# Kernel tuning notes

Hardware: AMD Instinct MI355X
Metric: run time of the kernel (lower is better)

The kernel has to match this reference:

```python
import jax, jax.numpy as jnp
import numpy as np

INPUT_SZ = 1024
HIDDEN_SZ = 1024


def setup_inputs() -> dict:
    key = jax.random.key(0)
    k1, k2, k3, k4, k5, k6 = jax.random.split(key, 6)
    s = 1.0 / np.sqrt(INPUT_SZ)
    x_batch = jax.random.normal(k1, (8, 2048, INPUT_SZ), dtype=jnp.float32)
    lin_w = jax.random.normal(k2, (INPUT_SZ, INPUT_SZ), dtype=jnp.float32) * s  # nn.Linear weight (out,in)
    lin_b = jax.random.normal(k3, (INPUT_SZ,), dtype=jnp.float32) * s
    W_q = jax.random.normal(k4, (INPUT_SZ, HIDDEN_SZ), dtype=jnp.float32) * s
    W_k = jax.random.normal(k5, (INPUT_SZ, HIDDEN_SZ), dtype=jnp.float32) * s
    W_v = jax.random.normal(k6, (INPUT_SZ, HIDDEN_SZ), dtype=jnp.float32) * s
    return {"x_batch": x_batch, "lin_w": lin_w, "lin_b": lin_b,
            "W_q": W_q, "W_k": W_k, "W_v": W_v}


def reference(x_batch, lin_w, lin_b, W_q, W_k, W_v):
    # x_batch: [B, S, D]. Prefill path (empty kv_cache of shape (2,)).
    B, S, D = x_batch.shape
    x = jnp.einsum('bsd,ed->bse', x_batch, lin_w) + lin_b  # nn.Linear: x @ W.T + b
    Q = jnp.einsum('bsd,dh->bsh', x, W_q)
    K = jnp.einsum('bsd,dh->bsh', x, W_k)
    V = jnp.einsum('bsd,dh->bsh', x, W_v)
    current_cache = jnp.stack([K, V])  # [2, B, S, H]
    I = jnp.einsum('bqh,bkh->bqk', Q, K)  # NOTE: no 1/sqrt(d) scaling, per original
    causal_mask = jnp.triu(jnp.ones((S, S), dtype=bool), k=1)  # True above diagonal
    I = jnp.where(causal_mask[None, :, :], -jnp.inf, I)
    F = jnp.einsum('bqk,bkh->bqh', jax.nn.softmax(I, axis=-1), V)
    return (F, current_cache)
```

## Files before the change

kernel.cpp:

```cpp
#include <hip/hip_runtime.h>
#include <cstdint>
#include <cstddef>


typedef short bf16x8 __attribute__((ext_vector_type(8)));
typedef float f32x4 __attribute__((ext_vector_type(4)));

__device__ __forceinline__ unsigned short f2bf(float f) {
    unsigned u = __float_as_uint(f);
    return (unsigned short)((u + 0x7fffu + ((u >> 16) & 1u)) >> 16);
}
__device__ __forceinline__ float bf2f(unsigned short h) {
    return __uint_as_float(((unsigned)h) << 16);
}

#define GLDS(gp, lp)                                                                \
    __builtin_amdgcn_global_load_lds((const __attribute__((address_space(1))) void*)(gp), \
                                     (__attribute__((address_space(3))) void*)(lp), 16, 0, 0)

#define PACK_BATCH ((size_t)136 * 16384)


__global__ __launch_bounds__(256)
void cvt_split(const float* __restrict__ in, unsigned short* __restrict__ h,
               unsigned short* __restrict__ l, size_t n4)
{
    size_t i = (size_t)blockIdx.x * blockDim.x + threadIdx.x;
    size_t stride = (size_t)gridDim.x * blockDim.x;
    for (; i < n4; i += stride) {
        float4 v = ((const float4*)in)[i];
        unsigned short h0 = f2bf(v.x), h1 = f2bf(v.y), h2 = f2bf(v.z), h3 = f2bf(v.w);
        uint2 hp, lp;
        hp.x = (unsigned)h0 | ((unsigned)h1 << 16);
        hp.y = (unsigned)h2 | ((unsigned)h3 << 16);
        lp.x = (unsigned)f2bf(v.x - bf2f(h0)) | ((unsigned)f2bf(v.y - bf2f(h1)) << 16);
        lp.y = (unsigned)f2bf(v.z - bf2f(h2)) | ((unsigned)f2bf(v.w - bf2f(h3)) << 16);
        ((uint2*)h)[i] = hp;
        ((uint2*)l)[i] = lp;
    }
}

template<bool PAIR>
__global__ __launch_bounds__(256)
void cvt_split_T(const float* __restrict__ in, unsigned short* __restrict__ hT,
                 unsigned short* __restrict__ lT, int R, int C,
                 size_t inBatch, size_t outBatch)
{
    __shared__ float tile[64][65];
    in += (size_t)blockIdx.z * inBatch;
    hT += (size_t)blockIdx.z * outBatch;
    const int c0 = blockIdx.x * 64, r0 = blockIdx.y * 64;
    const int tx = threadIdx.x & 63, ty = threadIdx.x >> 6;
    for (int i = ty; i < 64; i += 4)
        tile[i][tx] = in[(size_t)(r0 + i) * C + c0 + tx];
    __syncthreads();
    for (int i = ty; i < 64; i += 4) {
        float v = tile[tx][i];
        unsigned short hh = f2bf(v);
        size_t off = (size_t)(c0 + i) * R + r0 + tx;
        hT[off] = hh;
        if (PAIR) (lT + (size_t)blockIdx.z * outBatch)[off] = f2bf(v - bf2f(hh));
    }
}


template<bool SPLIT, bool BIAS, bool CMASK, bool CK, bool OUTF, bool OUTH, bool OUTL,
         bool PACKC, bool PACKA>
__global__ __launch_bounds__(256)
void gemm_bf16(const unsigned short* __restrict__ Ah, const unsigned short* __restrict__ Al,
               const unsigned short* __restrict__ Bh, const unsigned short* __restrict__ Bl,
               const float* __restrict__ bias,
               float* __restrict__ C, float* __restrict__ C7,
               unsigned short* __restrict__ Ch, unsigned short* __restrict__ Cl,
               int K, int ldA, int ldB, int ldC,
               size_t aBatch, size_t bBatch, size_t cBatch)
{
    const int row0 = blockIdx.y * 128, col0 = blockIdx.x * 128;
    if (CMASK && col0 > row0 + 127) return;

    const int bz = blockIdx.z;
    if (aBatch) { Ah += (size_t)bz * aBatch; if (SPLIT) Al += (size_t)bz * aBatch; }
    if (bBatch) { Bh += (size_t)bz * bBatch; if (SPLIT) Bl += (size_t)bz * bBatch; }
    if (cBatch) { C += (size_t)bz * cBatch; }

    extern __shared__ __align__(16) unsigned short sm[];
    unsigned short* sAh = sm;
    unsigned short* sBh = sm + 4096;
    unsigned short* sAl = sm + 8192;
    unsigned short* sBl = sm + 12288;

    const int t = threadIdx.x;
    const int wave = t >> 6, lane = t & 63;
    const int wr = wave >> 1, wc = wave & 1;
    const int mrow = lane & 15, kg = lane >> 4;

    int kEnd = K;
    if (CK) kEnd = min(K, row0 + 128);

    f32x4 acc[4][4] = {};

    const int c0 = wave * 2, c1 = wave * 2 + 1;
    size_t aOff0, aOff1;
    if (PACKA) {
        const int rblk = row0 >> 7;
        const size_t baseA = (((size_t)bz * 136) + (size_t)((rblk * (rblk + 1)) >> 1)) << 14;
        aOff0 = baseA + (size_t)(c0 * 16 + mrow) * 128 + kg * 8;
        aOff1 = baseA + (size_t)(c1 * 16 + mrow) * 128 + kg * 8;
    } else {
        aOff0 = (size_t)(row0 + c0 * 16 + mrow) * ldA + kg * 8;
        aOff1 = (size_t)(row0 + c1 * 16 + mrow) * ldA + kg * 8;
    }
    const size_t bOff0 = (size_t)(col0 + c0 * 16 + mrow) * ldB + kg * 8;
    const size_t bOff1 = (size_t)(col0 + c1 * 16 + mrow) * ldB + kg * 8;

    for (int k0 = 0; k0 < kEnd; k0 += 32) {
        const size_t aK = PACKA ? ((((size_t)(k0 >> 7)) << 14) | (size_t)(k0 & 127))
                                : (size_t)k0;
        GLDS(Ah + aOff0 + aK, sAh + c0 * 512);
        GLDS(Ah + aOff1 + aK, sAh + c1 * 512);
        GLDS(Bh + bOff0 + k0, sBh + c0 * 512);
        GLDS(Bh + bOff1 + k0, sBh + c1 * 512);
        if (SPLIT) {
            GLDS(Al + aOff0 + aK, sAl + c0 * 512);
            GLDS(Al + aOff1 + aK, sAl + c1 * 512);
            GLDS(Bl + bOff0 + k0, sBl + c0 * 512);
            GLDS(Bl + bOff1 + k0, sBl + c1 * 512);
        }
        __syncthreads();

        bf16x8 afh[4], bfh[4], afl[4], bfl[4];
        #pragma unroll
        for (int i = 0; i < 4; ++i) {
            afh[i] = *(const bf16x8*)(sAh + (wr * 4 + i) * 512 + lane * 8);
            bfh[i] = *(const bf16x8*)(sBh + (wc * 4 + i) * 512 + lane * 8);
            if (SPLIT) {
                afl[i] = *(const bf16x8*)(sAl + (wr * 4 + i) * 512 + lane * 8);
                bfl[i] = *(const bf16x8*)(sBl + (wc * 4 + i) * 512 + lane * 8);
            }
        }
        #pragma unroll
        for (int i = 0; i < 4; ++i)
            #pragma unroll
            for (int j = 0; j < 4; ++j) {
                acc[i][j] = __builtin_amdgcn_mfma_f32_16x16x32_bf16(afh[i], bfh[j], acc[i][j], 0, 0, 0);
                if (SPLIT) {
                    acc[i][j] = __builtin_amdgcn_mfma_f32_16x16x32_bf16(afh[i], bfl[j], acc[i][j], 0, 0, 0);
                    acc[i][j] = __builtin_amdgcn_mfma_f32_16x16x32_bf16(afl[i], bfh[j], acc[i][j], 0, 0, 0);
                }
            }
        __syncthreads();
    }

    float* Cout = C;
    size_t cbase = 0;
    if (PACKC) {
        const int rblk = row0 >> 7, cblk = col0 >> 7;
        Cout = (bz == 7) ? C7 : C + (size_t)bz * PACK_BATCH;
        cbase = ((size_t)((rblk * (rblk + 1)) >> 1) + (size_t)cblk) << 14;
    }
    const int rb = (lane >> 4) * 4;
    const int cl = lane & 15;
    #pragma unroll
    for (int j = 0; j < 4; ++j) {
        const int col = col0 + wc * 64 + j * 16 + cl;
        float bv = BIAS ? bias[col] : 0.f;
        #pragma unroll
        for (int i = 0; i < 4; ++i) {
            const int rw = row0 + wr * 64 + i * 16 + rb;
            #pragma unroll
            for (int r = 0; r < 4; ++r) {
                const int row = rw + r;
                float v = acc[i][j][r];
                if (BIAS) v += bv;
                if (CMASK && col > row) v = -__builtin_huge_valf();
                const size_t off = PACKC
                    ? (cbase + (size_t)(row - row0) * 128 + (size_t)(col - col0))
                    : ((size_t)row * ldC + col);
                if (OUTF) Cout[off] = v;
                if (OUTH) {
                    unsigned short hh = f2bf(v);
                    Ch[off] = hh;
                    if (OUTL) Cl[off] = f2bf(v - bf2f(hh));
                }
            }
        }
    }
}

__global__ __launch_bounds__(256)
void softmax_p_packed(const float* __restrict__ SF, const float* __restrict__ S7,
                      unsigned short* __restrict__ P)
{
    const int q = blockIdx.x, b = blockIdx.y;
    const int rblk = q >> 7, tri = (rblk * (rblk + 1)) >> 1;
    const size_t rowoff = ((size_t)tri << 14) + (size_t)(q & 127) * 128;
    const float* rowb = ((b == 7) ? S7 : SF + (size_t)b * PACK_BATCH) + rowoff;
    unsigned short* prow = P + (size_t)b * PACK_BATCH + rowoff;
    const int kend = rblk * 128 + 128;
    const int t = threadIdx.x;
    __shared__ float red[4];

    float m = -__builtin_huge_valf();
    for (int k = t; k < kend; k += 256)
        m = fmaxf(m, rowb[(((size_t)(k >> 7)) << 14) + (k & 127)]);
    #pragma unroll
    for (int off = 32; off; off >>= 1) m = fmaxf(m, __shfl_down(m, off, 64));
    if ((t & 63) == 0) red[t >> 6] = m;
    __syncthreads();
    m = fmaxf(fmaxf(red[0], red[1]), fmaxf(red[2], red[3]));
    __syncthreads();

    float e[8];
    float s = 0.f;
    int i = 0;
    for (int k = t; k < kend; k += 256, ++i) {
        float v = __expf(rowb[(((size_t)(k >> 7)) << 14) + (k & 127)] - m);
        e[i] = v;
        s += v;
    }
    #pragma unroll
    for (int off = 32; off; off >>= 1) s += __shfl_down(s, off, 64);
    if ((t & 63) == 0) red[t >> 6] = s;
    __syncthreads();
    s = red[0] + red[1] + red[2] + red[3];
    const float inv = 1.0f / s;
    i = 0;
    for (int k = t; k < kend; k += 256, ++i)
        prow[(((size_t)(k >> 7)) << 14) + (k & 127)] = f2bf(e[i] * inv);
}

#define TILE 64
#define KT 16
#define LDP (TILE + 4)
template<bool BT, bool BIAS, bool CMASK, bool CK>
__global__ __launch_bounds__(256)
void gemm_f32(const float* __restrict__ A, const float* __restrict__ B,
              const float* __restrict__ bias, float* __restrict__ C,
              int M, int N, int K, size_t sA, size_t sB, size_t sC)
{
    const int bm = blockIdx.y, bn = blockIdx.x;
    const int row0 = bm * TILE, col0 = bn * TILE;
    if (CMASK && col0 > row0 + (TILE - 1)) return;
    A += (size_t)blockIdx.z * sA; B += (size_t)blockIdx.z * sB; C += (size_t)blockIdx.z * sC;
    __shared__ float As[KT][LDP];
    __shared__ float Bs[KT][LDP];
    const int t = threadIdx.x;
    const int tx = t & 15, ty = t >> 4;
    const int lm = t >> 2, lk = (t & 3) << 2;
    int kEnd = K;
    if (CK) kEnd = min(K, row0 + TILE);
    float acc[4][4] = {};
    for (int k0 = 0; k0 < kEnd; k0 += KT) {
        {
            float4 a = *(const float4*)(A + (size_t)(row0 + lm) * K + (k0 + lk));
            As[lk + 0][lm] = a.x; As[lk + 1][lm] = a.y; As[lk + 2][lm] = a.z; As[lk + 3][lm] = a.w;
        }
        if (BT) {
            float4 b = *(const float4*)(B + (size_t)(col0 + lm) * K + (k0 + lk));
            Bs[lk + 0][lm] = b.x; Bs[lk + 1][lm] = b.y; Bs[lk + 2][lm] = b.z; Bs[lk + 3][lm] = b.w;
        } else {
            const int bk = t >> 4, bn4 = (t & 15) << 2;
            *(float4*)&Bs[bk][bn4] = *(const float4*)(B + (size_t)(k0 + bk) * N + (col0 + bn4));
        }
        __syncthreads();
        #pragma unroll
        for (int kk = 0; kk < KT; ++kk) {
            float av[4], bv[4];
            *(float4*)av = *(const float4*)&As[kk][ty << 2];
            *(float4*)bv = *(const float4*)&Bs[kk][tx << 2];
            #pragma unroll
            for (int i = 0; i < 4; ++i)
                #pragma unroll
                for (int j = 0; j < 4; ++j) acc[i][j] = fmaf(av[i], bv[j], acc[i][j]);
        }
        __syncthreads();
    }
    #pragma unroll
    for (int i = 0; i < 4; ++i) {
        const int r = row0 + (ty << 2) + i;
        float4 o; float* po = &o.x;
        #pragma unroll
        for (int j = 0; j < 4; ++j) {
            const int c = col0 + (tx << 2) + j;
            float v = acc[i][j];
            if (BIAS) v += bias[c];
            if (CMASK && c > r) v = -__builtin_huge_valf();
            po[j] = v;
        }
        *(float4*)(C + (size_t)r * N + col0 + (tx << 2)) = o;
    }
}
__global__ __launch_bounds__(256)
void softmax_causal(float* __restrict__ Sc, size_t batchStride, int ncols)
{
    const int q = blockIdx.x;
    float* row = Sc + (size_t)blockIdx.y * batchStride + (size_t)q * ncols;
    const int kend = (q & ~63) + 64;
    const int t = threadIdx.x;
    __shared__ float red[4];
    float m = -__builtin_huge_valf();
    for (int k = t; k < kend; k += 256) m = fmaxf(m, row[k]);
    #pragma unroll
    for (int off = 32; off; off >>= 1) m = fmaxf(m, __shfl_down(m, off, 64));
    if ((t & 63) == 0) red[t >> 6] = m;
    __syncthreads();
    m = fmaxf(fmaxf(red[0], red[1]), fmaxf(red[2], red[3]));
    __syncthreads();
    float e[8]; float s = 0.f; int i = 0;
    for (int k = t; k < kend; k += 256, ++i) { float v = __expf(row[k] - m); e[i] = v; s += v; }
    #pragma unroll
    for (int off = 32; off; off >>= 1) s += __shfl_down(s, off, 64);
    if ((t & 63) == 0) red[t >> 6] = s;
    __syncthreads();
    s = red[0] + red[1] + red[2] + red[3];
    const float inv = 1.0f / s;
    i = 0;
    for (int k = t; k < kend; k += 256, ++i) row[k] = e[i] * inv;
}


extern "C" void kernel_launch(void* const* d_in, const int* in_sizes, int n_in,
                              void* d_out, int out_size, void* d_ws, size_t ws_size,
                              hipStream_t stream)
{
    const float* x_batch = (const float*)d_in[0];
    const float* lin_w   = (const float*)d_in[1];
    const float* lin_b   = (const float*)d_in[2];
    const float* W_q     = (const float*)d_in[3];
    const float* W_k     = (const float*)d_in[4];
    const float* W_v     = (const float*)d_in[5];

    constexpr int Bn = 8, S = 2048, D = 1024;
    constexpr size_t MS = (size_t)Bn * S;
    constexpr size_t NE = MS * (size_t)D;
    constexpr size_t SB = (size_t)S * D;

    float* out = (float*)d_out;
    float* Fo = out;
    float* Kc = out + NE;
    float* Vc = out + 2 * NE;

    const size_t needFast = NE * 2 * 2ull
                          + NE * 2 * 2ull
                          + 14680064ull;

    if (ws_size >= needFast) {
        unsigned short* Qh  = (unsigned short*)d_ws;
        unsigned short* Ql  = Qh + NE;
        unsigned short* Kh  = Ql + NE;
        unsigned short* Kl  = Kh + NE;
        unsigned short* X   = Kl + NE;
        unsigned short* lwh = X,            *lwl = X + 1048576;
        unsigned short* wqh = X + 2097152,  *wql = X + 3145728;
        unsigned short* wkh = X + 4194304,  *wkl = X + 5242880;
        unsigned short* wvh = X + 6291456;
        float*          S7f = (float*)X;
        float*          SF  = Fo;
        unsigned short* Ph  = Qh;
        unsigned short* VhT = Kh;

        unsigned short* xbh = (unsigned short*)Kc;
        unsigned short* xbl = xbh + NE;
        unsigned short* xh  = (unsigned short*)Fo;
        unsigned short* xl  = xh + NE;

        const dim3 blk(256);

        cvt_split<<<4096, blk, 0, stream>>>(x_batch, xbh, xbl, NE / 4);
        cvt_split<<<512,  blk, 0, stream>>>(lin_w, lwh, lwl, (size_t)D * D / 4);
        cvt_split_T<true ><<<dim3(16, 16, 1), blk, 0, stream>>>(W_q, wqh, wql, D, D, 0, 0);
        cvt_split_T<true ><<<dim3(16, 16, 1), blk, 0, stream>>>(W_k, wkh, wkl, D, D, 0, 0);
        cvt_split_T<false><<<dim3(16, 16, 1), blk, 0, stream>>>(W_v, wvh, nullptr, D, D, 0, 0);

        const dim3 gBig(D / 128, MS / 128);

        gemm_bf16<true, true, false, false, false, true, true, false, false>
            <<<gBig, blk, 32768, stream>>>(xbh, xbl, lwh, lwl, lin_b,
                                           nullptr, nullptr, xh, xl, D, D, D, D, 0, 0, 0);
        gemm_bf16<true, false, false, false, false, true, true, false, false>
            <<<gBig, blk, 32768, stream>>>(xh, xl, wqh, wql, nullptr,
                                           nullptr, nullptr, Qh, Ql, D, D, D, D, 0, 0, 0);
        gemm_bf16<true, false, false, false, true, true, true, false, false>
            <<<gBig, blk, 32768, stream>>>(xh, xl, wkh, wkl, nullptr,
                                           Kc, nullptr, Kh, Kl, D, D, D, D, 0, 0, 0);
        gemm_bf16<false, false, false, false, true, false, false, false, false>
            <<<gBig, blk, 16384, stream>>>(xh, nullptr, wvh, nullptr, nullptr,
                                           Vc, nullptr, nullptr, nullptr, D, D, D, D, 0, 0, 0);

        gemm_bf16<true, false, true, false, true, false, false, true, false>
            <<<dim3(S / 128, S / 128, Bn), blk, 32768, stream>>>(
                Qh, Ql, Kh, Kl, nullptr,
                SF, S7f, nullptr, nullptr, D, D, D, 128, SB, SB, 0);

        softmax_p_packed<<<dim3(S, Bn), blk, 0, stream>>>(SF, S7f, Ph);

        cvt_split_T<false><<<dim3(D / 64, S / 64, Bn), blk, 0, stream>>>(
            Vc, VhT, nullptr, S, D, SB, SB);

        gemm_bf16<false, false, false, true, true, false, false, false, true>
            <<<dim3(D / 128, S / 128, Bn), blk, 16384, stream>>>(
                Ph, nullptr, VhT, nullptr, nullptr,
                Fo, nullptr, nullptr, nullptr, S, 128, S, D, 0, SB, SB);
    } else {
        float* x  = Fo;
        float* Q  = (float*)d_ws;
        float* Sc = Q + NE;
        const dim3 blk(256);
        const dim3 gBig(D / TILE, MS / TILE, 1);
        gemm_f32<true, true, false, false><<<gBig, blk, 0, stream>>>(
            x_batch, lin_w, lin_b, x, (int)MS, D, D, 0, 0, 0);
        gemm_f32<false, false, false, false><<<gBig, blk, 0, stream>>>(
            x, W_q, nullptr, Q, (int)MS, D, D, 0, 0, 0);
        gemm_f32<false, false, false, false><<<gBig, blk, 0, stream>>>(
            x, W_k, nullptr, Kc, (int)MS, D, D, 0, 0, 0);
        gemm_f32<false, false, false, false><<<gBig, blk, 0, stream>>>(
            x, W_v, nullptr, Vc, (int)MS, D, D, 0, 0, 0);
        for (int b = 0; b < Bn; ++b) {
            const float* Qb = Q  + (size_t)b * SB;
            const float* Kb = Kc + (size_t)b * SB;
            const float* Vb = Vc + (size_t)b * SB;
            float*       Fb = Fo + (size_t)b * SB;
            gemm_f32<true, false, true, false><<<dim3(S / TILE, S / TILE, 1), blk, 0, stream>>>(
                Qb, Kb, nullptr, Sc, S, S, D, 0, 0, 0);
            softmax_causal<<<dim3(S, 1, 1), blk, 0, stream>>>(Sc, 0, S);
            gemm_f32<false, false, false, true><<<dim3(D / TILE, S / TILE, 1), blk, 0, stream>>>(
                Sc, Vb, nullptr, Fb, S, D, S, 0, 0, 0);
        }
    }
}
```

Measured before the change: 1.247 ms.

## Add 256x256-tile GEMM kernel with triangular QK^T grid and XCD-aware block mapping

Introduces a new gemm256 kernel with 512 threads per block and 256x256 output tiles, double-buffered LDS staged via global_load_lds, and uses it for the input linear, the Q/K/V projections and the masked QK^T scores. The QK^T launch covers only lower-triangular tiles through a 1D grid decoded with a sqrt-based triangle index, and the projection GEMMs remap block IDs so consecutive tiles spread across chiplet groups. Larger tiles raise operand reuse per LDS load, but grids drop to 256 or 288 blocks, which may underfill the device. Each block also needs up to 128 KB of static shared memory and a large accumulator array, which adds register pressure.

Result: faster. 1.063 ms (-14.8%).

```diff
diff --git a/kernel.cpp b/kernel.cpp
--- a/kernel.cpp
+++ b/kernel.cpp
@@ -1,6 +1,7 @@
 #include <hip/hip_runtime.h>
 #include <cstdint>
 #include <cstddef>
+#include <cmath>
 
 
 typedef short bf16x8 __attribute__((ext_vector_type(8)));
@@ -64,6 +65,138 @@
 }
 
 
+template<bool SPLIT, bool BIAS, bool QKT, bool OUTF, bool OUTH, bool OUTL>
+__global__ __launch_bounds__(512, 2)
+void gemm256(const unsigned short* __restrict__ Ah, const unsigned short* __restrict__ Al,
+             const unsigned short* __restrict__ Bh, const unsigned short* __restrict__ Bl,
+             const float* __restrict__ bias,
+             float* __restrict__ C, float* __restrict__ C7,
+             unsigned short* __restrict__ Ch, unsigned short* __restrict__ Cl,
+             int K, int ldA, int ldB, int ldC, int nbx,
+             size_t aBatch, size_t bBatch)
+{
+    int row0, col0, batch = 0;
+    if (QKT) {
+        const int bid = blockIdx.x;
+        batch = bid & 7;
+        const int ti = bid >> 3;
+        int r = (int)((sqrtf(8.f * (float)ti + 1.f) - 1.f) * 0.5f);
+        while (((r + 1) * (r + 2)) / 2 <= ti) ++r;
+        while ((r * (r + 1)) / 2 > ti) --r;
+        const int c = ti - (r * (r + 1)) / 2;
+        row0 = r * 256; col0 = c * 256;
+        Ah += (size_t)batch * aBatch; Bh += (size_t)batch * bBatch;
+        if (SPLIT) { Al += (size_t)batch * aBatch; Bl += (size_t)batch * bBatch; }
+    } else {
+        const int bid = blockIdx.x;
+        const int chunk = gridDim.x >> 3;
+        const int lb = (bid & 7) * chunk + (bid >> 3);
+        row0 = (lb / nbx) * 256; col0 = (lb % nbx) * 256;
+    }
+
+    constexpr int PL = 8192;
+    constexpr int BUF = SPLIT ? 32768 : 16384;
+    __shared__ unsigned short sm[SPLIT ? 65536 : 32768];
+
+    const int t = threadIdx.x, wave = t >> 6, lane = t & 63;
+    const int wr = wave >> 2, wc = wave & 3;
+    const int mrow = lane & 15, kg = lane >> 4;
+    const int c0 = wave * 2, c1 = wave * 2 + 1;
+
+    const size_t aOff0 = (size_t)(row0 + c0 * 16 + mrow) * ldA + kg * 8;
+    const size_t aOff1 = (size_t)(row0 + c1 * 16 + mrow) * ldA + kg * 8;
+    const size_t bOff0 = (size_t)(col0 + c0 * 16 + mrow) * ldB + kg * 8;
+    const size_t bOff1 = (size_t)(col0 + c1 * 16 + mrow) * ldB + kg * 8;
+
+    f32x4 acc[8][4] = {};
+    const int nt = K / 32;
+
+#define STAGE256(step, bb)                                                   \
+    do {                                                                     \
+        unsigned short* db = sm + (bb);                                      \
+        const size_t kof = (size_t)(step) * 32;                              \
+        GLDS(Ah + aOff0 + kof, db + c0 * 512);                               \
+        GLDS(Ah + aOff1 + kof, db + c1 * 512);                               \
+        GLDS(Bh + bOff0 + kof, db + (SPLIT ? 2 * PL : PL) + c0 * 512);       \
+        GLDS(Bh + bOff1 + kof, db + (SPLIT ? 2 * PL : PL) + c1 * 512);       \
+        if (SPLIT) {                                                         \
+            GLDS(Al + aOff0 + kof, db + PL + c0 * 512);                      \
+            GLDS(Al + aOff1 + kof, db + PL + c1 * 512);                      \
+            GLDS(Bl + bOff0 + kof, db + 3 * PL + c0 * 512);                  \
+            GLDS(Bl + bOff1 + kof, db + 3 * PL + c1 * 512);                  \
+        }                                                                    \
+    } while (0)
+
+    STAGE256(0, 0);
+    __syncthreads();
+
+    for (int ts = 0; ts < nt; ++ts) {
+        unsigned short* sb = sm + (ts & 1) * BUF;
+        if (ts + 1 < nt) STAGE256(ts + 1, ((ts + 1) & 1) * BUF);
+        bf16x8 bh[4], bl[4];
+        #pragma unroll
+        for (int j = 0; j < 4; ++j) {
+            bh[j] = *(const bf16x8*)(sb + (SPLIT ? 2 * PL : PL) + (wc * 4 + j) * 512 + lane * 8);
+            if (SPLIT) bl[j] = *(const bf16x8*)(sb + 3 * PL + (wc * 4 + j) * 512 + lane * 8);
+        }
+        #pragma unroll
+        for (int i = 0; i < 8; ++i) {
+            bf16x8 ah = *(const bf16x8*)(sb + (wr * 8 + i) * 512 + lane * 8);
+            bf16x8 al;
+            if (SPLIT) al = *(const bf16x8*)(sb + PL + (wr * 8 + i) * 512 + lane * 8);
+            __builtin_amdgcn_s_setprio(1);
+            #pragma unroll
+            for (int j = 0; j < 4; ++j) {
+                acc[i][j] = __builtin_amdgcn_mfma_f32_16x16x32_bf16(ah, bh[j], acc[i][j], 0, 0, 0);
+                if (SPLIT) {
+                    acc[i][j] = __builtin_amdgcn_mfma_f32_16x16x32_bf16(ah, bl[j], acc[i][j], 0, 0, 0);
+                    acc[i][j] = __builtin_amdgcn_mfma_f32_16x16x32_bf16(al, bh[j], acc[i][j], 0, 0, 0);
+                }
+            }
+            __builtin_amdgcn_s_setprio(0);
+        }
+        __syncthreads();
+    }
+#undef STAGE256
+
+    float* Cout = C;
+    if (QKT) Cout = (batch == 7) ? C7 : C + (size_t)batch * PACK_BATCH;
+    const int rb = (lane >> 4) * 4, cl = lane & 15;
+    #pragma unroll
+    for (int j = 0; j < 4; ++j) {
+        const int col = col0 + wc * 64 + j * 16 + cl;
+        const float bv = BIAS ? bias[col] : 0.f;
+        #pragma unroll
+        for (int i = 0; i < 8; ++i) {
+            const int rw = row0 + wr * 128 + i * 16 + rb;
+            #pragma unroll
+            for (int r = 0; r < 4; ++r) {
+                const int row = rw + r;
+                float v = acc[i][j][r];
+                if (BIAS) v += bv;
+                if (QKT) {
+                    if (col > row) v = -__builtin_huge_valf();
+                    const int rblk = row >> 7, cblk = col >> 7;
+                    if (rblk >= cblk) {
+                        const size_t off = ((size_t)(((rblk * (rblk + 1)) >> 1) + cblk) << 14)
+                                         + ((size_t)(row & 127) << 7) + (size_t)(col & 127);
+                        Cout[off] = v;
+                    }
+                } else {
+                    const size_t off = (size_t)row * ldC + col;
+                    if (OUTF) Cout[off] = v;
+                    if (OUTH) {
+                        unsigned short hh = f2bf(v);
+                        Ch[off] = hh;
+                        if (OUTL) Cl[off] = f2bf(v - bf2f(hh));
+                    }
+                }
+            }
+        }
+    }
+}
+
+
 template<bool SPLIT, bool BIAS, bool CMASK, bool CK, bool OUTF, bool OUTH, bool OUTL,
          bool PACKC, bool PACKA>
 __global__ __launch_bounds__(256)
@@ -83,11 +216,11 @@
     if (bBatch) { Bh += (size_t)bz * bBatch; if (SPLIT) Bl += (size_t)bz * bBatch; }
     if (cBatch) { C += (size_t)bz * cBatch; }
 
-    extern __shared__ __align__(16) unsigned short sm[];
-    unsigned short* sAh = sm;
-    unsigned short* sBh = sm + 4096;
-    unsigned short* sAl = sm + 8192;
-    unsigned short* sBl = sm + 12288;
+    extern __shared__ __align__(16) unsigned short smd[];
+    unsigned short* sAh = smd;
+    unsigned short* sBh = smd + 4096;
+    unsigned short* sAl = smd + 8192;
+    unsigned short* sBl = smd + 12288;
 
     const int t = threadIdx.x;
     const int wave = t >> 6, lane = t & 63;
@@ -365,6 +498,7 @@
         unsigned short* xl  = xh + NE;
 
         const dim3 blk(256);
+        const dim3 blk512(512);
 
         cvt_split<<<4096, blk, 0, stream>>>(x_batch, xbh, xbl, NE / 4);
         cvt_split<<<512,  blk, 0, stream>>>(lin_w, lwh, lwl, (size_t)D * D / 4);
@@ -372,25 +506,19 @@
         cvt_split_T<true ><<<dim3(16, 16, 1), blk, 0, stream>>>(W_k, wkh, wkl, D, D, 0, 0);
         cvt_split_T<false><<<dim3(16, 16, 1), blk, 0, stream>>>(W_v, wvh, nullptr, D, D, 0, 0);
 
-        const dim3 gBig(D / 128, MS / 128);
-
-        gemm_bf16<true, true, false, false, false, true, true, false, false>
-            <<<gBig, blk, 32768, stream>>>(xbh, xbl, lwh, lwl, lin_b,
-                                           nullptr, nullptr, xh, xl, D, D, D, D, 0, 0, 0);
-        gemm_bf16<true, false, false, false, false, true, true, false, false>
-            <<<gBig, blk, 32768, stream>>>(xh, xl, wqh, wql, nullptr,
-                                           nullptr, nullptr, Qh, Ql, D, D, D, D, 0, 0, 0);
-        gemm_bf16<true, false, false, false, true, true, true, false, false>
-            <<<gBig, blk, 32768, stream>>>(xh, xl, wkh, wkl, nullptr,
-                                           Kc, nullptr, Kh, Kl, D, D, D, D, 0, 0, 0);
-        gemm_bf16<false, false, false, false, true, false, false, false, false>
-            <<<gBig, blk, 16384, stream>>>(xh, nullptr, wvh, nullptr, nullptr,
-                                           Vc, nullptr, nullptr, nullptr, D, D, D, D, 0, 0, 0);
-
-        gemm_bf16<true, false, true, false, true, false, false, true, false>
-            <<<dim3(S / 128, S / 128, Bn), blk, 32768, stream>>>(
-                Qh, Ql, Kh, Kl, nullptr,
-                SF, S7f, nullptr, nullptr, D, D, D, 128, SB, SB, 0);
+        gemm256<true, true, false, false, true, true><<<dim3(256), blk512, 0, stream>>>(
+            xbh, xbl, lwh, lwl, lin_b, nullptr, nullptr, xh, xl, D, D, D, D, 4, 0, 0);
+        gemm256<true, false, false, false, true, true><<<dim3(256), blk512, 0, stream>>>(
+            xh, xl, wqh, wql, nullptr, nullptr, nullptr, Qh, Ql, D, D, D, D, 4, 0, 0);
+        gemm256<true, false, false, true, true, true><<<dim3(256), blk512, 0, stream>>>(
+            xh, xl, wkh, wkl, nullptr, Kc, nullptr, Kh, Kl, D, D, D, D, 4, 0, 0);
+        gemm256<false, false, false, true, false, false><<<dim3(256), blk512, 0, stream>>>(
+            xh, nullptr, wvh, nullptr, nullptr, Vc, nullptr, nullptr, nullptr,
+            D, D, D, D, 4, 0, 0);
+
+        gemm256<true, false, true, true, false, false><<<dim3(288), blk512, 0, stream>>>(
+            Qh, Ql, Kh, Kl, nullptr, SF, S7f, nullptr, nullptr,
+            D, D, D, 128, 1, SB, SB);
 
         softmax_p_packed<<<dim3(S, Bn), blk, 0, stream>>>(SF, S7f, Ph);
 
```
